# Optimization experiments

Hardware: AMD Instinct MI355X
Metric: run time of the kernel (lower is better)

## Reference

```python
import jax, jax.numpy as jnp
import numpy as np


def setup_inputs() -> dict:
    key = jax.random.key(0)
    ks = jax.random.split(key, 8)
    B, T, F, H, O = 512, 128, 512, 512, 256
    s = 0.05
    return {
        "states": jax.random.normal(ks[0], (B, T, F), jnp.float32),
        "terminated": jax.random.bernoulli(ks[1], 0.02, (B, T)),
        "h0": jnp.zeros((B, H), jnp.float32),
        "W_ih": jax.random.normal(ks[2], (H, F), jnp.float32) * s,
        "W_hh": jax.random.normal(ks[3], (H, H), jnp.float32) * s,
        "b_ih": jax.random.normal(ks[4], (H,), jnp.float32) * s,
        "b_hh": jax.random.normal(ks[5], (H,), jnp.float32) * s,
        "fc_w": jax.random.normal(ks[6], (O, H), jnp.float32) * s,
        "fc_b": jax.random.normal(ks[7], (O,), jnp.float32) * s,
    }


def reference(states, terminated, h0, W_ih, W_hh, b_ih, b_hh, fc_w, fc_b):
    # states: [B, T, F]; terminated: [B, T] bool; h0: [B, H] (num_layers=1)
    B, T, F = states.shape
    # Precompute the input projection once (big GEMM outside the scan).
    x_proj = jnp.einsum("btf,hf->bth", states, W_ih) + b_ih + b_hh  # [B, T, H]
    x_proj_t = jnp.swapaxes(x_proj, 0, 1)          # [T, B, H]
    term_t = jnp.swapaxes(terminated, 0, 1)        # [T, B]

    def step(h, inp):
        xp, tm = inp                               # xp: [B, H], tm: [B]
        h_new = jnp.tanh(xp + h @ W_hh.T)          # vanilla RNN (tanh) cell
        # Zero hidden state of envs that terminated at this step (applied
        # AFTER emitting the output, matching the torch segment-reset logic).
        h_next = jnp.where(tm[:, None], jnp.zeros_like(h_new), h_new)
        return h_next, h_new

    h_final, outs = jax.lax.scan(step, h0, (x_proj_t, term_t))  # outs: [T, B, H]
    rnn_output = jnp.swapaxes(outs, 0, 1).reshape(B * T, -1)    # [B*T, H]
    logits = rnn_output @ fc_w.T + fc_b                          # [B*T, O]
    return logits, h_final
```

## Files before the change

### kernel.cpp

```cpp
#include <hip/hip_runtime.h>
#include <hip/hip_bf16.h>
#include <hip/hip_fp16.h>


typedef _Float16 half8 __attribute__((ext_vector_type(8)));
typedef _Float16 half4 __attribute__((ext_vector_type(4)));
typedef float f32x4 __attribute__((ext_vector_type(4)));

#define XPW_OFF   0UL
#define WIH_OFF   67108864UL
#define FCW_OFF   67633152UL
#define BIAS_OFF  67895296UL
#define WRESA_OFF 67897344UL
#define WRESL_OFF 68290560UL

#define LDS_BARRIER()                                              \
    do {                                                           \
        __builtin_amdgcn_sched_barrier(0);                         \
        asm volatile("s_waitcnt lgkmcnt(0)" ::: "memory");         \
        __builtin_amdgcn_s_barrier();                              \
        __builtin_amdgcn_sched_barrier(0);                         \
    } while (0)


__global__ void conv_w(const float* __restrict__ Wih, const float* __restrict__ Whh,
                       const float* __restrict__ fcw, const float* __restrict__ bih,
                       const float* __restrict__ bhh,
                       _Float16* __restrict__ wih_h, _Float16* __restrict__ fcw_h,
                       float* __restrict__ bias2,
                       _Float16* __restrict__ wresA, _Float16* __restrict__ wresL) {
    int idx = blockIdx.x * 256 + threadIdx.x;
    if (idx < 262144) wih_h[idx] = (_Float16)Wih[idx];
    if (idx < 196608) {
        const int i = idx & 7, l = (idx >> 3) & 63, s = (idx >> 9) & 15;
        const int rest = idx >> 13;
        const int w = rest / 3, nt = rest % 3;
        const int ntg = nt * 8 + w;
        wresA[idx] = (_Float16)Whh[(size_t)(ntg * 16 + (l & 15)) * 512 + s * 32 + (l >> 4) * 8 + i];
    }
    if (idx < 65536) {
        const int i = idx & 7, l = (idx >> 3) & 63, s = (idx >> 9) & 15, w = idx >> 13;
        const int ntg = 24 + w;
        wresL[idx] = (_Float16)Whh[(size_t)(ntg * 16 + (l & 15)) * 512 + s * 32 + (l >> 4) * 8 + i];
    }
    if (idx < 131072) fcw_h[idx] = (_Float16)fcw[idx];
    if (idx < 512) bias2[idx] = bih[idx] + bhh[idx];
}

__global__ __launch_bounds__(256) void gemm_xproj(const float* __restrict__ A,
                                                  const _Float16* __restrict__ Bw,
                                                  const float* __restrict__ bias2,
                                                  _Float16* __restrict__ out) {
    __shared__ _Float16 As[128 * 32];
    __shared__ _Float16 Bs[64 * 32];
    const int tid = threadIdx.x;
    const int s_ = blockIdx.x;
    const int z = s_ & 7, k_ = s_ >> 3;
    const int gid = z * 512 + k_;
    const int b = gid >> 3;
    const int wsp = gid & 7;
    const int lane = tid & 63, w1 = tid >> 6;
    const int ln = lane & 15, kg = lane >> 4;

    f32x4 acc[2][4];
#pragma unroll
    for (int m = 0; m < 2; m++)
#pragma unroll
        for (int n = 0; n < 4; n++) acc[m][n] = (f32x4)0.0f;

    const int sr = tid >> 1, sc = (tid & 1) * 16;
    const int sr2 = tid >> 2, sc2 = (tid & 3) * 8;
    const int brow = (sr2 >> 4) * 128 + wsp * 16 + (sr2 & 15);

    for (int k0 = 0; k0 < 512; k0 += 32) {
        {
            const float* ga = A + (size_t)(b * 128 + sr) * 512 + k0 + sc;
            float4 f0 = *(const float4*)(ga + 0);
            float4 f1 = *(const float4*)(ga + 4);
            float4 f2 = *(const float4*)(ga + 8);
            float4 f3 = *(const float4*)(ga + 12);
            half8 h0, h1;
            h0[0] = (_Float16)f0.x; h0[1] = (_Float16)f0.y; h0[2] = (_Float16)f0.z; h0[3] = (_Float16)f0.w;
            h0[4] = (_Float16)f1.x; h0[5] = (_Float16)f1.y; h0[6] = (_Float16)f1.z; h0[7] = (_Float16)f1.w;
            h1[0] = (_Float16)f2.x; h1[1] = (_Float16)f2.y; h1[2] = (_Float16)f2.z; h1[3] = (_Float16)f2.w;
            h1[4] = (_Float16)f3.x; h1[5] = (_Float16)f3.y; h1[6] = (_Float16)f3.z; h1[7] = (_Float16)f3.w;
            *(half8*)&As[sr * 32 + sc] = h0;
            *(half8*)&As[sr * 32 + sc + 8] = h1;
        }
        *(half8*)&Bs[sr2 * 32 + sc2] = *(const half8*)(Bw + (size_t)brow * 512 + k0 + sc2);
        __syncthreads();
        half8 af[2], bf[4];
#pragma unroll
        for (int m = 0; m < 2; m++) af[m] = *(const half8*)&As[(w1 * 32 + m * 16 + ln) * 32 + kg * 8];
#pragma unroll
        for (int n = 0; n < 4; n++) bf[n] = *(const half8*)&Bs[(n * 16 + ln) * 32 + kg * 8];
#pragma unroll
        for (int m = 0; m < 2; m++)
#pragma unroll
            for (int n = 0; n < 4; n++)
                acc[m][n] = __builtin_amdgcn_mfma_f32_16x16x32_f16(af[m], bf[n], acc[m][n], 0, 0, 0);
        __syncthreads();
    }
    const int bg = b >> 4, kgs = (b >> 2) & 3, qs = b & 3;
    float bv[4];
#pragma unroll
    for (int n = 0; n < 4; n++) bv[n] = bias2[(n * 8 + wsp) * 16 + ln];
    const size_t tb = (size_t)(bg * 128) * 8192 + (size_t)(wsp * 64 + kgs * 16 + ln) * 16 + qs * 4;
#pragma unroll
    for (int m = 0; m < 2; m++)
#pragma unroll
        for (int q = 0; q < 4; q++) {
            half4 v;
#pragma unroll
            for (int n = 0; n < 4; n++) v[n] = (_Float16)(acc[m][n][q] + bv[n]);
            const int t = w1 * 32 + m * 16 + kg * 4 + q;
            *(half4*)&out[tb + (size_t)t * 8192] = v;
        }
}

__global__ __launch_bounds__(512, 2) void rnn_scan14(
    const _Float16* __restrict__ xps,
    const _Float16* __restrict__ wresA,
    const _Float16* __restrict__ wresL,
    const int* __restrict__ term,
    const float* __restrict__ h0,
    float* dout) {
    __shared__ __align__(16) _Float16 hb[8192];
    __shared__ __align__(16) _Float16 wl[65536];
    __shared__ unsigned int term_lds[16][4];
    const int tid = threadIdx.x;
    const int bg = blockIdx.x;
    const int R0 = bg * 16;
    const int lane = tid & 63, w = tid >> 6;
    const int ln = lane & 15, kg = lane >> 4;
    _Float16* rnn = (_Float16*)dout;

    half8 wf[48];
    {
        const _Float16* wp = wresA + (size_t)w * 24576 + lane * 8;
#pragma unroll
        for (int f = 0; f < 48; f++) wf[f] = *(const half8*)(wp + (size_t)f * 512);
    }
#pragma unroll
    for (int f = 0; f < 48; f++) asm volatile("" : "+a"(wf[f]));

    for (int u = 0; u < 16; u++) {
        const int o = (u * 512 + tid) * 8;
        *(half8*)&wl[o] = *(const half8*)(wresL + o);
    }
    {
        const int r = tid >> 5, c0 = (tid & 31) * 16;
        const float* gh = h0 + (size_t)(R0 + r) * 512 + c0;
        half8 v0, v1;
#pragma unroll
        for (int i = 0; i < 8; i++) { v0[i] = (_Float16)gh[i]; v1[i] = (_Float16)gh[8 + i]; }
        const int kb = c0 >> 3;
        *(half8*)&hb[kb * 128 + r * 8] = v0;
        *(half8*)&hb[(kb + 1) * 128 + r * 8] = v1;
    }
    if (tid < 64) {
        const int r = tid >> 2, word = tid & 3;
        unsigned int m = 0;
        for (int b2 = 0; b2 < 32; b2++)
            m |= (term[(R0 + r) * 128 + word * 32 + b2] ? 1u : 0u) << b2;
        term_lds[r][word] = m;
    }
    __syncthreads();

    const _Float16* xpt = xps + (size_t)(bg * 128) * 8192 + tid * 16;
    const _Float16* bl = &wl[(size_t)w * 8192];
    unsigned int tmask[4];

#pragma unroll 1
    for (int t = 0; t < 128; ++t) {
        if ((t & 31) == 0) {
#pragma unroll
            for (int q = 0; q < 4; q++) tmask[q] = term_lds[kg * 4 + q][t >> 5];
        }
        const half8 xv0 = *(const half8*)(xpt);
        const half8 xv1 = *(const half8*)(xpt + 8);
        xpt += 8192;

        f32x4 acc[4];
#pragma unroll
        for (int n = 0; n < 4; n++) acc[n] = (f32x4)0.0f;

#pragma unroll
        for (int s = 0; s < 16; s++) {
            const half8 a = *(const half8*)&hb[(s * 4 + kg) * 128 + ln * 8];
            acc[0] = __builtin_amdgcn_mfma_f32_16x16x32_f16(a, wf[s],      acc[0], 0, 0, 0);
            acc[1] = __builtin_amdgcn_mfma_f32_16x16x32_f16(a, wf[16 + s], acc[1], 0, 0, 0);
            acc[2] = __builtin_amdgcn_mfma_f32_16x16x32_f16(a, wf[32 + s], acc[2], 0, 0, 0);
            const half8 b4 = *(const half8*)(bl + s * 512 + lane * 8);
            acc[3] = __builtin_amdgcn_mfma_f32_16x16x32_f16(a, b4, acc[3], 0, 0, 0);
        }
        LDS_BARRIER();

        _Float16 hh[16];
#pragma unroll
        for (int q = 0; q < 4; q++)
#pragma unroll
            for (int nt = 0; nt < 4; nt++) {
                const int u = q * 4 + nt;
                const float xval = (float)(u < 8 ? xv0[u] : xv1[u - 8]);
                const float pre = acc[nt][q] + xval;
                const float e = __expf(2.0f * pre);
                const float hn = 1.0f - 2.0f * __builtin_amdgcn_rcpf(e + 1.0f);
                hh[q * 4 + nt] = (_Float16)hn;
                const int c = (nt * 8 + w) * 16 + ln;
                hb[(c >> 3) * 128 + (kg * 4 + q) * 8 + (c & 7)] =
                    ((tmask[q] >> (t & 31)) & 1) ? (_Float16)0.0f : hh[q * 4 + nt];
            }
        LDS_BARRIER();

#pragma unroll
        for (int q = 0; q < 4; q++)
#pragma unroll
            for (int nt = 0; nt < 4; nt++) {
                const int c = (nt * 8 + w) * 16 + ln;
                rnn[(size_t)((R0 + kg * 4 + q) * 128 + t) * 512 + c] = hh[q * 4 + nt];
            }
    }

    {
        const int r = tid >> 5, c0 = (tid & 31) * 16;
        const int kb = c0 >> 3;
        half8 v0 = *(const half8*)&hb[kb * 128 + r * 8];
        half8 v1 = *(const half8*)&hb[(kb + 1) * 128 + r * 8];
        float* gf = dout + (size_t)65536 * 256 + (size_t)(R0 + r) * 512 + c0;
#pragma unroll
        for (int i = 0; i < 8; i++) { gf[i] = (float)v0[i]; gf[8 + i] = (float)v1[i]; }
    }
}

__global__ __launch_bounds__(512) void gemm_logits(const _Float16* Arnn,
                                                   const _Float16* __restrict__ Bw,
                                                   const float* __restrict__ biasv,
                                                   float* out) {
    __shared__ _Float16 As[128 * 32];
    __shared__ _Float16 Bs[256 * 32];
    const int tid = threadIdx.x;
    const int m0 = blockIdx.x * 128;
    const int lane = tid & 63, w = tid >> 6;
    const int wr = (w >> 2) * 64, wc = (w & 3) * 64;
    const int ln = lane & 15, kg = lane >> 4;

    f32x4 acc[4][4];
#pragma unroll
    for (int m = 0; m < 4; m++)
#pragma unroll
        for (int n = 0; n < 4; n++) acc[m][n] = (f32x4)0.0f;

    const int ar = tid >> 2, ac = (tid & 3) * 8;
    const int br = tid >> 1, bc = (tid & 1) * 16;

    for (int k0 = 0; k0 < 512; k0 += 32) {
        *(half8*)&As[ar * 32 + ac] = *(const half8*)(Arnn + (size_t)(m0 + ar) * 512 + k0 + ac);
        {
            const _Float16* gb = Bw + (size_t)br * 512 + k0 + bc;
            *(half8*)&Bs[br * 32 + bc] = *(const half8*)(gb);
            *(half8*)&Bs[br * 32 + bc + 8] = *(const half8*)(gb + 8);
        }
        __syncthreads();
        half8 af[4], bf[4];
#pragma unroll
        for (int m = 0; m < 4; m++) af[m] = *(const half8*)&As[(wr + m * 16 + ln) * 32 + kg * 8];
#pragma unroll
        for (int n = 0; n < 4; n++) bf[n] = *(const half8*)&Bs[(wc + n * 16 + ln) * 32 + kg * 8];
#pragma unroll
        for (int m = 0; m < 4; m++)
#pragma unroll
            for (int n = 0; n < 4; n++)
                acc[m][n] = __builtin_amdgcn_mfma_f32_16x16x32_f16(af[m], bf[n], acc[m][n], 0, 0, 0);
        __syncthreads();
    }
#pragma unroll
    for (int m = 0; m < 4; m++)
#pragma unroll
        for (int n = 0; n < 4; n++) {
            const int col = wc + n * 16 + ln;
            const float bv = biasv[col];
#pragma unroll
            for (int q = 0; q < 4; q++) {
                const int row = m0 + wr + m * 16 + kg * 4 + q;
                out[(size_t)row * 256 + col] = acc[m][n][q] + bv;
            }
        }
}

extern "C" void kernel_launch(void* const* d_in, const int* in_sizes, int n_in,
                              void* d_out, int out_size, void* d_ws, size_t ws_size,
                              hipStream_t stream) {
    const float* states = (const float*)d_in[0];
    const int*   term   = (const int*)d_in[1];
    const float* h0     = (const float*)d_in[2];
    const float* Wih    = (const float*)d_in[3];
    const float* Whh    = (const float*)d_in[4];
    const float* bih    = (const float*)d_in[5];
    const float* bhh    = (const float*)d_in[6];
    const float* fcw    = (const float*)d_in[7];
    const float* fcb    = (const float*)d_in[8];

    char* ws = (char*)d_ws;
    _Float16* xpw   = (_Float16*)(ws + XPW_OFF);
    _Float16* wih_h = (_Float16*)(ws + WIH_OFF);
    _Float16* fcw_h = (_Float16*)(ws + FCW_OFF);
    float*    bias2 = (float*)(ws + BIAS_OFF);
    _Float16* wresA = (_Float16*)(ws + WRESA_OFF);
    _Float16* wresL = (_Float16*)(ws + WRESL_OFF);

    conv_w<<<1024, 256, 0, stream>>>(Wih, Whh, fcw, bih, bhh, wih_h, fcw_h, bias2, wresA, wresL);
    gemm_xproj<<<4096, 256, 0, stream>>>(states, wih_h, bias2, xpw);
    rnn_scan14<<<32, 512, 0, stream>>>(xpw, wresA, wresL, term, h0, (float*)d_out);
    gemm_logits<<<512, 512, 0, stream>>>((const _Float16*)d_out, fcw_h, fcb, (float*)d_out);
}
```

Before: 478.5 us.

## Remap hidden-unit ownership so scan writes contiguous half4 stores

The W_hh rows are permuted so that each lane in the recurrent scan owns four consecutive hidden units rather than units strided by 128. The scan can then write the hidden state into LDS and the rnn output to global memory as half4 vectors instead of scalar fp16 stores. The xproj GEMM is remapped to match this column ordering, and its epilogue now stages results through LDS so the global writes are coalesced. The cost is extra LDS usage and a barrier in the xproj kernel, plus possible LDS bank conflicts from the new access pattern.

```diff
diff --git a/kernel.cpp b/kernel.cpp
--- a/kernel.cpp
+++ b/kernel.cpp
@@ -13,6 +13,7 @@
 #define BIAS_OFF  67895296UL
 #define WRESA_OFF 67897344UL
 #define WRESL_OFF 68290560UL
+
 
 #define LDS_BARRIER()                                              \
     do {                                                           \
@@ -21,7 +22,6 @@
         __builtin_amdgcn_s_barrier();                              \
         __builtin_amdgcn_sched_barrier(0);                         \
     } while (0)
-
 
 __global__ void conv_w(const float* __restrict__ Wih, const float* __restrict__ Whh,
                        const float* __restrict__ fcw, const float* __restrict__ bih,
@@ -35,13 +35,13 @@
         const int i = idx & 7, l = (idx >> 3) & 63, s = (idx >> 9) & 15;
         const int rest = idx >> 13;
         const int w = rest / 3, nt = rest % 3;
-        const int ntg = nt * 8 + w;
-        wresA[idx] = (_Float16)Whh[(size_t)(ntg * 16 + (l & 15)) * 512 + s * 32 + (l >> 4) * 8 + i];
+        const int row = w * 64 + (l & 15) * 4 + nt;
+        wresA[idx] = (_Float16)Whh[(size_t)row * 512 + s * 32 + (l >> 4) * 8 + i];
     }
     if (idx < 65536) {
         const int i = idx & 7, l = (idx >> 3) & 63, s = (idx >> 9) & 15, w = idx >> 13;
-        const int ntg = 24 + w;
-        wresL[idx] = (_Float16)Whh[(size_t)(ntg * 16 + (l & 15)) * 512 + s * 32 + (l >> 4) * 8 + i];
+        const int row = w * 64 + (l & 15) * 4 + 3;
+        wresL[idx] = (_Float16)Whh[(size_t)row * 512 + s * 32 + (l >> 4) * 8 + i];
     }
     if (idx < 131072) fcw_h[idx] = (_Float16)fcw[idx];
     if (idx < 512) bias2[idx] = bih[idx] + bhh[idx];
@@ -53,6 +53,7 @@
                                                   _Float16* __restrict__ out) {
     __shared__ _Float16 As[128 * 32];
     __shared__ _Float16 Bs[64 * 32];
+    __shared__ _Float16 ep[128 * 64];
     const int tid = threadIdx.x;
     const int s_ = blockIdx.x;
     const int z = s_ & 7, k_ = s_ >> 3;
@@ -70,7 +71,7 @@
 
     const int sr = tid >> 1, sc = (tid & 1) * 16;
     const int sr2 = tid >> 2, sc2 = (tid & 3) * 8;
-    const int brow = (sr2 >> 4) * 128 + wsp * 16 + (sr2 & 15);
+    const int brow = wsp * 64 + sr2;
 
     for (int k0 = 0; k0 < 512; k0 += 32) {
         {
@@ -101,24 +102,31 @@
                 acc[m][n] = __builtin_amdgcn_mfma_f32_16x16x32_f16(af[m], bf[n], acc[m][n], 0, 0, 0);
         __syncthreads();
     }
+    float bv[4];
+#pragma unroll
+    for (int n = 0; n < 4; n++) bv[n] = bias2[wsp * 64 + n * 16 + ln];
+#pragma unroll
+    for (int m = 0; m < 2; m++)
+#pragma unroll
+        for (int q = 0; q < 4; q++) {
+            const int t = w1 * 32 + m * 16 + kg * 4 + q;
+#pragma unroll
+            for (int n = 0; n < 4; n++)
+                ep[t * 64 + n * 16 + ln] = (_Float16)(acc[m][n][q] + bv[n]);
+        }
+    __syncthreads();
     const int bg = b >> 4, kgs = (b >> 2) & 3, qs = b & 3;
-    float bv[4];
-#pragma unroll
-    for (int n = 0; n < 4; n++) bv[n] = bias2[(n * 8 + wsp) * 16 + ln];
-    const size_t tb = (size_t)(bg * 128) * 8192 + (size_t)(wsp * 64 + kgs * 16 + ln) * 16 + qs * 4;
-#pragma unroll
-    for (int m = 0; m < 2; m++)
-#pragma unroll
-        for (int q = 0; q < 4; q++) {
-            half4 v;
-#pragma unroll
-            for (int n = 0; n < 4; n++) v[n] = (_Float16)(acc[m][n][q] + bv[n]);
-            const int t = w1 * 32 + m * 16 + kg * 4 + q;
-            *(half4*)&out[tb + (size_t)t * 8192] = v;
-        }
-}
-
-__global__ __launch_bounds__(512, 2) void rnn_scan14(
+    const size_t obase = (size_t)(bg * 128) * 8192 + (size_t)(wsp * 64 + kgs * 16) * 16 + qs * 4;
+#pragma unroll
+    for (int j = 0; j < 8; j++) {
+        const int wid = tid * 8 + j;
+        const int t2 = wid >> 4, sln = wid & 15;
+        const half4 v = *(const half4*)&ep[t2 * 64 + sln * 4];
+        *(half4*)&out[obase + (size_t)t2 * 8192 + sln * 16] = v;
+    }
+}
+
+__global__ __launch_bounds__(512, 2) void rnn_scan15(
     const _Float16* __restrict__ xps,
     const _Float16* __restrict__ wresA,
     const _Float16* __restrict__ wresL,
@@ -169,6 +177,8 @@
 
     const _Float16* xpt = xps + (size_t)(bg * 128) * 8192 + tid * 16;
     const _Float16* bl = &wl[(size_t)w * 8192];
+    const int cb = w * 64 + ln * 4;
+    const int hoff = (cb >> 3) * 128 + (cb & 7);
     unsigned int tmask[4];
 
 #pragma unroll 1
@@ -196,30 +206,29 @@
         }
         LDS_BARRIER();
 
-        _Float16 hh[16];
-#pragma unroll
-        for (int q = 0; q < 4; q++)
+        half4 hh4[4];
+#pragma unroll
+        for (int q = 0; q < 4; q++) {
+            const bool dead = (tmask[q] >> (t & 31)) & 1;
+            half4 v;
 #pragma unroll
             for (int nt = 0; nt < 4; nt++) {
                 const int u = q * 4 + nt;
                 const float xval = (float)(u < 8 ? xv0[u] : xv1[u - 8]);
                 const float pre = acc[nt][q] + xval;
                 const float e = __expf(2.0f * pre);
-                const float hn = 1.0f - 2.0f * __builtin_amdgcn_rcpf(e + 1.0f);
-                hh[q * 4 + nt] = (_Float16)hn;
-                const int c = (nt * 8 + w) * 16 + ln;
-                hb[(c >> 3) * 128 + (kg * 4 + q) * 8 + (c & 7)] =
-                    ((tmask[q] >> (t & 31)) & 1) ? (_Float16)0.0f : hh[q * 4 + nt];
+                v[nt] = (_Float16)(1.0f - 2.0f * __builtin_amdgcn_rcpf(e + 1.0f));
             }
+            hh4[q] = v;
+            half4 mv = v;
+            if (dead) { mv[0] = (_Float16)0; mv[1] = (_Float16)0; mv[2] = (_Float16)0; mv[3] = (_Float16)0; }
+            *(half4*)&hb[hoff + (kg * 4 + q) * 8] = mv;
+        }
         LDS_BARRIER();
 
 #pragma unroll
         for (int q = 0; q < 4; q++)
-#pragma unroll
-            for (int nt = 0; nt < 4; nt++) {
-                const int c = (nt * 8 + w) * 16 + ln;
-                rnn[(size_t)((R0 + kg * 4 + q) * 128 + t) * 512 + c] = hh[q * 4 + nt];
-            }
+            *(half4*)&rnn[((size_t)(R0 + kg * 4 + q) * 128 + t) * 512 + cb] = hh4[q];
     }
 
     {
@@ -311,6 +320,6 @@
 
     conv_w<<<1024, 256, 0, stream>>>(Wih, Whh, fcw, bih, bhh, wih_h, fcw_h, bias2, wresA, wresL);
     gemm_xproj<<<4096, 256, 0, stream>>>(states, wih_h, bias2, xpw);
-    rnn_scan14<<<32, 512, 0, stream>>>(xpw, wresA, wresL, term, h0, (float*)d_out);
+    rnn_scan15<<<32, 512, 0, stream>>>(xpw, wresA, wresL, term, h0, (float*)d_out);
     gemm_logits<<<512, 512, 0, stream>>>((const _Float16*)d_out, fcw_h, fcb, (float*)d_out);
 }
```

Measured after the change: 429.8 us. 1.11x faster.
